# Kernel optimization log

Hardware: AMD Instinct MI355X
Metric: run time of the kernel (lower is better)

Reference implementation:

```python
import jax, jax.numpy as jnp
import numpy as np

# config (matches SS2Dv2 defaults: d_model=96, d_state=16, ssm_ratio=2.0, dt_rank=auto=6, k_group=4)
DM, DI, N, K, R = 96, 192, 16, 4, 6
BSZ, H_, W_ = 1, 56, 56


def setup_inputs() -> dict:
    key = jax.random.key(0)
    ks = jax.random.split(key, 8)
    return {
        "x": jax.random.normal(ks[0], (BSZ, H_, W_, DM), jnp.float32),
        "in_proj_w": jax.random.normal(ks[1], (2 * DI, DM), jnp.float32) / np.sqrt(DM).astype(np.float32),
        "conv_w": jax.random.normal(ks[2], (DI, 1, 3, 3), jnp.float32) * 0.1,
        "conv_b": jnp.zeros((DI,), jnp.float32),
        "x_proj_w": jax.random.normal(ks[3], (K, R + 2 * N, DI), jnp.float32) / np.sqrt(DI).astype(np.float32),
        "dt_projs_w": 0.1 * jax.random.uniform(ks[4], (K, DI, R), jnp.float32),
        "dt_projs_bias": 0.1 * jax.random.uniform(ks[5], (K, DI), jnp.float32),
        "A_logs": jnp.zeros((K * DI, N), jnp.float32),
        "Ds": jnp.ones((K * DI,), jnp.float32),
        "ln_w": jnp.ones((DI,), jnp.float32),
        "ln_b": jnp.zeros((DI,), jnp.float32),
        "out_proj_w": jax.random.normal(ks[6], (DM, DI), jnp.float32) / np.sqrt(DI).astype(np.float32),
    }


def _cross_scan(x):
    # x: (B, D, H, W) -> (B, 4, D, L); dirs: row-major, col-major, and their flips
    B, D, H, W = x.shape
    L = H * W
    x0 = x.reshape(B, D, L)
    x1 = jnp.swapaxes(x, 2, 3).reshape(B, D, L)
    return jnp.stack([x0, x1, x0[..., ::-1], x1[..., ::-1]], axis=1)


def _cross_merge(ys, H, W):
    # ys: (B, K, D, L) -> (B, D, L); invert each scan direction and sum
    B, Kk, D, L = ys.shape
    y0 = ys[:, 0]
    y2 = ys[:, 2][..., ::-1]
    y1 = jnp.swapaxes(ys[:, 1].reshape(B, D, W, H), 2, 3).reshape(B, D, L)
    y3 = jnp.swapaxes(ys[:, 3][..., ::-1].reshape(B, D, W, H), 2, 3).reshape(B, D, L)
    return y0 + y1 + y2 + y3


def _forward(x, in_proj_w, conv_w, conv_b, x_proj_w, dt_projs_w, dt_projs_bias,
             A_logs, Ds, ln_w, ln_b, out_proj_w):
    B, H, W, _ = x.shape
    L = H * W
    # in_proj + gate split (channel_first=False -> last dim)
    xz = jnp.einsum('bhwc,oc->bhwo', x, in_proj_w)
    xc, z = jnp.split(xz, 2, axis=-1)
    z = jax.nn.silu(z)
    # depthwise conv (NCHW)
    xc = jnp.transpose(xc, (0, 3, 1, 2))
    xc = jax.lax.conv_general_dilated(
        xc, conv_w, (1, 1), 'SAME', feature_group_count=DI,
        dimension_numbers=('NCHW', 'OIHW', 'NCHW')) + conv_b[None, :, None, None]
    xc = jax.nn.silu(xc)
    # 4-directional cross scan
    xs = _cross_scan(xc)  # (B,K,D,L)
    # grouped x_proj: per direction D -> R+2N
    x_dbl = jnp.einsum('bkdl,krd->bkrl', xs, x_proj_w)
    dts, Bs, Cs = jnp.split(x_dbl, [R, R + N], axis=2)  # (B,K,R,L),(B,K,N,L),(B,K,N,L)
    # grouped dt proj: per direction R -> D
    dts = jnp.einsum('bkrl,kdr->bkdl', dts, dt_projs_w)
    A = -jnp.exp(A_logs.astype(jnp.float32)).reshape(K, DI, N)
    delta = jax.nn.softplus(dts + dt_projs_bias[None, :, :, None])  # (B,K,D,L)
    # S6 selective scan: h_t = exp(delta*A)*h_{t-1} + delta*B*u, y_t = C.h_t + D*u
    dA = jnp.exp(jnp.einsum('bkdl,kdn->bkdln', delta, A))
    dBu = jnp.einsum('bkdl,bknl,bkdl->bkdln', delta, Bs, xs)

    def comb(e1, e2):
        a1, b1 = e1
        a2, b2 = e2
        return a2 * a1, a2 * b1 + b2

    _, h = jax.lax.associative_scan(comb, (dA, dBu), axis=3)  # (B,K,D,L,N)
    y = jnp.einsum('bkdln,bknl->bkdl', h, Cs) + Ds.reshape(K, DI)[None, :, :, None] * xs
    y = _cross_merge(y, H, W).reshape(B, DI, H, W)
    # out_norm: LayerNorm over channels (channel_first=False path)
    y = jnp.transpose(y, (0, 2, 3, 1))  # (B,H,W,D)
    mu = y.mean(-1, keepdims=True)
    var = ((y - mu) ** 2).mean(-1, keepdims=True)
    y = (y - mu) / jnp.sqrt(var + 1e-5) * ln_w + ln_b
    y = y * z
    return jnp.einsum('bhwd,od->bhwo', y, out_proj_w)


def reference(x, in_proj_w, conv_w, conv_b, x_proj_w, dt_projs_w, dt_projs_bias,
              A_logs, Ds, ln_w, ln_b, out_proj_w):
    return _forward(x, in_proj_w, conv_w, conv_b, x_proj_w, dt_projs_w, dt_projs_bias,
                    A_logs, Ds, ln_w, ln_b, out_proj_w)
```

## Files before the change

### kernel.cpp

```cpp
#include <hip/hip_runtime.h>
#include <hip/hip_bf16.h>
#include <math.h>

#define DM 96
#define DI 192
#define NS 16
#define KK 4
#define RR 6
#define HH 56
#define WW 56
#define LL (HH*WW)
#define RN (RR + 2*NS)
#define NCH 64
#define CLL (LL/NCH)

__device__ __forceinline__ float silu_f(float x) { return x / (1.f + __expf(-x)); }
__device__ __forceinline__ float softplus_f(float x) {
    return (x > 20.f) ? x : log1pf(__expf(x));
}

__global__ __launch_bounds__(256) void k_inproj(
        const float* __restrict__ x, const float* __restrict__ w,
        float* __restrict__ xc_t, float* __restrict__ z_nat) {
    __shared__ float xt[64 * 100];
    __shared__ float wt[32 * 100];
    const int l0 = blockIdx.x * 64;
    const int o0 = blockIdx.y * 32;
    const int tid = threadIdx.x;
    for (int i = tid; i < 64 * 96; i += 256) {
        int r = i / 96, c = i % 96;
        xt[r * 100 + c] = x[(size_t)(l0 + r) * DM + c];
    }
    for (int i = tid; i < 32 * 96; i += 256) {
        int r = i / 96, c = i % 96;
        wt[r * 100 + c] = w[(size_t)(o0 + r) * DM + c];
    }
    __syncthreads();
    const int tx = tid & 15, ty = tid >> 4;
    float acc[4][2] = {};
    for (int c = 0; c < 96; c += 4) {
        float4 av[4], bv[2];
#pragma unroll
        for (int i = 0; i < 4; ++i) av[i] = *(const float4*)&xt[(ty + 16 * i) * 100 + c];
#pragma unroll
        for (int j = 0; j < 2; ++j) bv[j] = *(const float4*)&wt[(tx + 16 * j) * 100 + c];
#pragma unroll
        for (int i = 0; i < 4; ++i)
#pragma unroll
            for (int j = 0; j < 2; ++j) {
                acc[i][j] = fmaf(av[i].x, bv[j].x, acc[i][j]);
                acc[i][j] = fmaf(av[i].y, bv[j].y, acc[i][j]);
                acc[i][j] = fmaf(av[i].z, bv[j].z, acc[i][j]);
                acc[i][j] = fmaf(av[i].w, bv[j].w, acc[i][j]);
            }
    }
    __syncthreads();
    float* ot = xt;
#pragma unroll
    for (int j = 0; j < 2; ++j)
#pragma unroll
        for (int i = 0; i < 4; ++i)
            ot[(tx + 16 * j) * 65 + (ty + 16 * i)] = acc[i][j];
    __syncthreads();
    if (o0 < DI) {
        for (int i = tid; i < 32 * 64; i += 256) {
            int ol = i >> 6, ll = i & 63;
            xc_t[(size_t)(o0 + ol) * LL + l0 + ll] = ot[ol * 65 + ll];
        }
    } else {
        for (int i = tid; i < 32 * 64; i += 256) {
            int ll = i >> 5, ol = i & 31;
            z_nat[(size_t)(l0 + ll) * DI + (o0 - DI) + ol] = silu_f(ot[ol * 65 + ll]);
        }
    }
}

__global__ __launch_bounds__(256) void k_convT(
        const float* __restrict__ xc_t, const float* __restrict__ cw,
        const float* __restrict__ cb, float* __restrict__ xconv, float* __restrict__ xs1) {
    __shared__ float in_s[16 * 56];
    __shared__ float out_s[14 * 57];
    const int d = blockIdx.x;
    const int h0 = blockIdx.y * 14;
    const int tid = threadIdx.x;
    const float* in = xc_t + (size_t)d * LL;
    for (int i = tid; i < 16 * 56; i += 256) {
        int r = i / 56 - 1 + h0;
        int cpos = i % 56;
        in_s[i] = (r >= 0 && r < HH) ? in[r * WW + cpos] : 0.f;
    }
    __syncthreads();
    const float b0 = cb[d];
    float w9[9];
#pragma unroll
    for (int i = 0; i < 9; ++i) w9[i] = cw[d * 9 + i];
    for (int i = tid; i < 14 * 56; i += 256) {
        int hh = i / 56, w = i % 56;
        float acc = b0;
#pragma unroll
        for (int di = 0; di < 3; ++di)
#pragma unroll
            for (int dj = 0; dj < 3; ++dj) {
                int w2 = w + dj - 1;
                if (w2 < 0 || w2 >= WW) continue;
                acc = fmaf(in_s[(hh + di) * 56 + w2], w9[di * 3 + dj], acc);
            }
        acc = silu_f(acc);
        xconv[(size_t)d * LL + (h0 + hh) * WW + w] = acc;
        out_s[hh * 57 + w] = acc;
    }
    __syncthreads();
    for (int i = tid; i < 14 * 56; i += 256) {
        int w = i / 14, hh = i % 14;
        xs1[(size_t)d * LL + w * HH + h0 + hh] = out_s[hh * 57 + w];
    }
}

__global__ __launch_bounds__(256) void k_xdblD(
        const float* __restrict__ xconv, const float* __restrict__ xs1,
        const float* __restrict__ pw, const float* __restrict__ dtw,
        const float* __restrict__ dtb,
        float* __restrict__ Bn, float* __restrict__ Cn, float* __restrict__ delta) {
    __shared__ float xt[DI * 32];
    __shared__ float wk_s[32 * DI];
    __shared__ float dtS[RR * 33];
    const int k = blockIdx.y;
    const int l0 = blockIdx.x * 32;
    const int tid = threadIdx.x;
    const float* in = (k & 1) ? xs1 : xconv;
    const float* wk = pw + (size_t)k * RN * DI;
    for (int i = tid; i < DI * 32; i += 256) {
        int d = i >> 5, lx = i & 31;
        xt[i] = in[(size_t)d * LL + l0 + lx];
    }
    {
        const float4* src = (const float4*)(wk + RR * DI);
        float4* dst = (float4*)wk_s;
        for (int i = tid; i < (32 * DI) / 4; i += 256) dst[i] = src[i];
    }
    __syncthreads();
    if (tid < RR * 32) {
        int r = tid >> 5, lx = tid & 31;
        const float* wr = wk + r * DI;
        float acc = 0.f;
#pragma unroll 8
        for (int d = 0; d < DI; ++d) acc = fmaf(xt[(d << 5) + lx], wr[d], acc);
        dtS[r * 33 + lx] = acc;
    }
    {
        const int sx = tid & 31, cg = tid >> 5;
        float acc4[4] = {};
        for (int d = 0; d < DI; d += 4) {
            float x0 = xt[(d + 0) * 32 + sx];
            float x1 = xt[(d + 1) * 32 + sx];
            float x2 = xt[(d + 2) * 32 + sx];
            float x3 = xt[(d + 3) * 32 + sx];
#pragma unroll
            for (int j = 0; j < 4; ++j) {
                float4 wv = *(const float4*)&wk_s[(cg + 8 * j) * DI + d];
                acc4[j] = fmaf(x0, wv.x, acc4[j]);
                acc4[j] = fmaf(x1, wv.y, acc4[j]);
                acc4[j] = fmaf(x2, wv.z, acc4[j]);
                acc4[j] = fmaf(x3, wv.w, acc4[j]);
            }
        }
        int s = l0 + sx;
#pragma unroll
        for (int j = 0; j < 4; ++j) {
            int col = cg + 8 * j;
            if (col < NS) Bn[((size_t)k * LL + s) * NS + col] = acc4[j];
            else          Cn[((size_t)k * LL + s) * NS + (col - NS)] = acc4[j];
        }
    }
    __syncthreads();
    for (int oi = tid; oi < DI * 32; oi += 256) {
        int d = oi >> 5, sl = oi & 31;
        int kd = k * DI + d;
        const float* wr = dtw + (size_t)kd * RR;
        float acc = dtb[kd];
#pragma unroll
        for (int r = 0; r < RR; ++r) acc = fmaf(dtS[r * 33 + sl], wr[r], acc);
        delta[(size_t)kd * LL + l0 + sl] = softplus_f(acc);
    }
}

template<int STP, bool TRANS>
__device__ __forceinline__ void scan_dir(
        const float* __restrict__ pd, const float* __restrict__ pu,
        const float* __restrict__ pB, const float* __restrict__ pC,
        float An, float Dv, int c, int n,
        float* __restrict__ sP, float* __restrict__ sH,
        float* __restrict__ yo0,
        float* __restrict__ ysm,
        int im0) {
    float sd = 0.f, h = 0.f;
#pragma unroll 7
    for (int tl = 0; tl < CLL; ++tl) {
        float dl = pd[STP * tl];
        float u  = pu[STP * tl];
        float Bv = pB[STP * NS * tl];
        float dA = __expf(dl * An);
        h = fmaf(dA, h, dl * Bv * u);
        sd += dl;
    }
    sP[c * NS + n] = __expf(sd * An);
    sH[c * NS + n] = h;
    __syncthreads();
    float hin = 0.f;
    for (int cc = 0; cc < c; ++cc)
        hin = fmaf(sP[cc * NS + n], hin, sH[cc * NS + n]);

    float h2 = hin;
    float yreg[4];
#pragma unroll 7
    for (int tl = 0; tl < CLL; ++tl) {
        float dl = pd[STP * tl];
        float u  = pu[STP * tl];
        float Bv = pB[STP * NS * tl];
        float Cv = pC[STP * NS * tl];
        float dA = __expf(dl * An);
        h2 = fmaf(dA, h2, dl * Bv * u);
        float acc = h2 * Cv;
        acc += __shfl_xor(acc, 8, 64);
        acc += __shfl_xor(acc, 4, 64);
        acc += __shfl_xor(acc, 2, 64);
        acc += __shfl_xor(acc, 1, 64);
        acc = fmaf(Dv, u, acc);
        if ((tl & 15) == n) yreg[tl >> 4] = acc;
    }
    if (!TRANS) {
#pragma unroll
        for (int j = 0; j < 3; ++j)
            yo0[STP * (j * 16 + n)] = yreg[j];
        if (n == 0)
            yo0[STP * 48] = yreg[3];
    } else {
#pragma unroll
        for (int j = 0; j < 3; ++j) {
            int im = im0 + STP * (j * 16 + n);
            int w = im / HH, hh = im - w * HH;
            ysm[hh * 57 + w] = yreg[j];
        }
        if (n == 0) {
            int im = im0 + STP * 48;
            int w = im / HH, hh = im - w * HH;
            ysm[hh * 57 + w] = yreg[3];
        }
    }
}

__global__ __launch_bounds__(1024) void k_scan(
        const float* __restrict__ delta, const float* __restrict__ Bn,
        const float* __restrict__ Cn,
        const float* __restrict__ xconv, const float* __restrict__ xs1,
        const float* __restrict__ A_logs, const float* __restrict__ Ds,
        float* __restrict__ y4) {
    __shared__ float sP[NCH * NS];
    __shared__ float sH[NCH * NS];
    __shared__ float ys[HH * 57];
    int b = blockIdx.x;
    int k = b / DI, d = b % DI;
    int tid = threadIdx.x;
    int c = tid >> 4, n = tid & 15;
    int kd = k * DI + d;
    float An = -__expf(A_logs[kd * NS + n]);
    float Dv = Ds[kd];
    const float* del = delta + (size_t)kd * LL;
    const float* uP  = ((k & 1) ? xs1 : xconv) + (size_t)d * LL;
    const float* Bb  = Bn + (size_t)k * LL * NS;
    const float* Cb  = Cn + (size_t)k * LL * NS;
    float* yo = y4 + (size_t)kd * LL;
    const int t0 = c * CLL;
    const int imF = t0;
    const int imR = LL - 1 - t0;
    if (k == 0) {
        scan_dir<1, false>(del + imF, uP + imF,
                           Bb + (size_t)imF * NS + n, Cb + (size_t)imF * NS + n,
                           An, Dv, c, n, sP, sH, yo + imF, nullptr, 0);
    } else if (k == 1) {
        scan_dir<1, true>(del + imF, uP + imF,
                          Bb + (size_t)imF * NS + n, Cb + (size_t)imF * NS + n,
                          An, Dv, c, n, sP, sH, nullptr, ys, imF);
    } else if (k == 2) {
        scan_dir<-1, false>(del + imR, uP + imR,
                            Bb + (size_t)imR * NS + n, Cb + (size_t)imR * NS + n,
                            An, Dv, c, n, sP, sH, yo + imR, nullptr, 0);
    } else {
        scan_dir<-1, true>(del + imR, uP + imR,
                           Bb + (size_t)imR * NS + n, Cb + (size_t)imR * NS + n,
                           An, Dv, c, n, sP, sH, nullptr, ys, imR);
    }
    if (k & 1) {
        __syncthreads();
        for (int p = tid; p < LL; p += 1024)
            yo[p] = ys[p + p / WW];
    }
}

__global__ __launch_bounds__(256) void k_lnout(
        const float* __restrict__ y4, const float* __restrict__ z_nat,
        const float* __restrict__ lnw, const float* __restrict__ lnb,
        const float* __restrict__ ow, float* __restrict__ out) {
    __shared__ float yv[32 * 196];
    __shared__ float ow_s[48 * 196];
    __shared__ float mean_s[32], inv_s[32];
    const int l0 = blockIdx.x * 32;
    const int pass = blockIdx.y;
    const int tid = threadIdx.x;
    for (int i = tid; i < DI * 32; i += 256) {
        int d = i >> 5, p = i & 31;
        size_t off = (size_t)d * LL + l0 + p;
        float v = y4[off]
                + y4[(size_t)DI * LL + off]
                + y4[(size_t)(2 * DI) * LL + off]
                + y4[(size_t)(3 * DI) * LL + off];
        yv[p * 196 + d] = v;
    }
    __syncthreads();
    {
        int p = tid >> 3, e = tid & 7;
        float s1 = 0.f;
#pragma unroll
        for (int m = 0; m < 24; ++m) s1 += yv[p * 196 + e + 8 * m];
        s1 += __shfl_xor(s1, 4, 64);
        s1 += __shfl_xor(s1, 2, 64);
        s1 += __shfl_xor(s1, 1, 64);
        float mean = s1 * (1.f / DI);
        float s2 = 0.f;
#pragma unroll
        for (int m = 0; m < 24; ++m) {
            float dv = yv[p * 196 + e + 8 * m] - mean;
            s2 = fmaf(dv, dv, s2);
        }
        s2 += __shfl_xor(s2, 4, 64);
        s2 += __shfl_xor(s2, 2, 64);
        s2 += __shfl_xor(s2, 1, 64);
        if (e == 0) {
            mean_s[p] = mean;
            inv_s[p] = rsqrtf(s2 * (1.f / DI) + 1e-5f);
        }
    }
    __syncthreads();
    for (int i = tid; i < DI * 32; i += 256) {
        int p = i / DI, d = i % DI;
        float yn = (yv[p * 196 + d] - mean_s[p]) * inv_s[p] * lnw[d] + lnb[d];
        yv[p * 196 + d] = yn * z_nat[(size_t)(l0 + p) * DI + d];
    }
    for (int i = tid; i < 48 * DI; i += 256) {
        int o = i / DI, dd = i % DI;
        ow_s[o * 196 + dd] = ow[(size_t)(pass * 48 + o) * DI + dd];
    }
    __syncthreads();
    const int ty = tid >> 4, tx = tid & 15;
    float acc[2][3] = {};
    for (int dd = 0; dd < DI; dd += 4) {
        float4 a0 = *(const float4*)&yv[(ty * 2 + 0) * 196 + dd];
        float4 a1 = *(const float4*)&yv[(ty * 2 + 1) * 196 + dd];
#pragma unroll
        for (int j = 0; j < 3; ++j) {
            float4 bv = *(const float4*)&ow_s[(tx + 16 * j) * 196 + dd];
            acc[0][j] += a0.x * bv.x + a0.y * bv.y + a0.z * bv.z + a0.w * bv.w;
            acc[1][j] += a1.x * bv.x + a1.y * bv.y + a1.z * bv.z + a1.w * bv.w;
        }
    }
#pragma unroll
    for (int il = 0; il < 2; ++il)
#pragma unroll
        for (int j = 0; j < 3; ++j)
            out[(size_t)(l0 + ty * 2 + il) * DM + pass * 48 + tx + 16 * j] = acc[il][j];
}

extern "C" void kernel_launch(void* const* d_in, const int* in_sizes, int n_in,
                              void* d_out, int out_size, void* d_ws, size_t ws_size,
                              hipStream_t stream) {
    const float* x    = (const float*)d_in[0];
    const float* ipw  = (const float*)d_in[1];
    const float* cw   = (const float*)d_in[2];
    const float* cb   = (const float*)d_in[3];
    const float* xpw  = (const float*)d_in[4];
    const float* dtw  = (const float*)d_in[5];
    const float* dtb  = (const float*)d_in[6];
    const float* alog = (const float*)d_in[7];
    const float* Dsp  = (const float*)d_in[8];
    const float* lnw  = (const float*)d_in[9];
    const float* lnb  = (const float*)d_in[10];
    const float* ow   = (const float*)d_in[11];
    float* out = (float*)d_out;

    float* ws     = (float*)d_ws;
    float* xc_t   = ws;
    float* z_nat  = xc_t + DI * LL;
    float* xconv  = z_nat + DI * LL;
    float* xs1    = xconv + DI * LL;
    float* Bn     = xs1 + DI * LL;
    float* Cn     = Bn + (size_t)KK * LL * NS;
    float* delta  = Cn + (size_t)KK * LL * NS;
    float* y4     = delta + (size_t)KK * DI * LL;

    k_inproj <<<dim3(LL / 64, 12), 256, 0, stream>>>(x, ipw, xc_t, z_nat);
    k_convT  <<<dim3(DI, 4), 256, 0, stream>>>(xc_t, cw, cb, xconv, xs1);
    k_xdblD  <<<dim3(LL / 32, KK), 256, 0, stream>>>(xconv, xs1, xpw, dtw, dtb, Bn, Cn, delta);
    k_scan   <<<KK * DI, 1024, 0, stream>>>(delta, Bn, Cn, xconv, xs1, alog, Dsp, y4);
    k_lnout  <<<dim3(LL / 32, 2), 256, 0, stream>>>(y4, z_nat, lnw, lnb, ow, out);
}
```

Baseline: 187.7 us.

## Store delta/B/C chunk-major in scan order and vectorize global loads

```diff
diff --git a/kernel.cpp b/kernel.cpp
--- a/kernel.cpp
+++ b/kernel.cpp
@@ -12,7 +12,8 @@
 #define LL (HH*WW)
 #define RN (RR + 2*NS)
 #define NCH 64
-#define CLL (LL/NCH)
+#define CLL 49
+#define CPAD 52
 
 __device__ __forceinline__ float silu_f(float x) { return x / (1.f + __expf(-x)); }
 __device__ __forceinline__ float softplus_f(float x) {
@@ -27,13 +28,13 @@
     const int l0 = blockIdx.x * 64;
     const int o0 = blockIdx.y * 32;
     const int tid = threadIdx.x;
-    for (int i = tid; i < 64 * 96; i += 256) {
-        int r = i / 96, c = i % 96;
-        xt[r * 100 + c] = x[(size_t)(l0 + r) * DM + c];
-    }
-    for (int i = tid; i < 32 * 96; i += 256) {
-        int r = i / 96, c = i % 96;
-        wt[r * 100 + c] = w[(size_t)(o0 + r) * DM + c];
+    for (int i = tid; i < 64 * 24; i += 256) {
+        int r = i / 24, q = i % 24;
+        *(float4*)&xt[r * 100 + 4 * q] = *(const float4*)&x[(size_t)(l0 + r) * DM + 4 * q];
+    }
+    for (int i = tid; i < 32 * 24; i += 256) {
+        int r = i / 24, q = i % 24;
+        *(float4*)&wt[r * 100 + 4 * q] = *(const float4*)&w[(size_t)(o0 + r) * DM + 4 * q];
     }
     __syncthreads();
     const int tx = tid & 15, ty = tid >> 4;
@@ -84,10 +85,12 @@
     const int h0 = blockIdx.y * 14;
     const int tid = threadIdx.x;
     const float* in = xc_t + (size_t)d * LL;
-    for (int i = tid; i < 16 * 56; i += 256) {
-        int r = i / 56 - 1 + h0;
-        int cpos = i % 56;
-        in_s[i] = (r >= 0 && r < HH) ? in[r * WW + cpos] : 0.f;
+    for (int i = tid; i < 16 * 14; i += 256) {
+        int row = i / 14, q = i % 14;
+        int r = row - 1 + h0;
+        float4 v = make_float4(0.f, 0.f, 0.f, 0.f);
+        if (r >= 0 && r < HH) v = *(const float4*)&in[r * WW + 4 * q];
+        *(float4*)&in_s[row * 56 + 4 * q] = v;
     }
     __syncthreads();
     const float b0 = cb[d];
@@ -120,7 +123,7 @@
         const float* __restrict__ xconv, const float* __restrict__ xs1,
         const float* __restrict__ pw, const float* __restrict__ dtw,
         const float* __restrict__ dtb,
-        float* __restrict__ Bn, float* __restrict__ Cn, float* __restrict__ delta) {
+        float* __restrict__ Bt, float* __restrict__ Ct, float* __restrict__ delta_cm) {
     __shared__ float xt[DI * 32];
     __shared__ float wk_s[32 * DI];
     __shared__ float dtS[RR * 33];
@@ -129,9 +132,9 @@
     const int tid = threadIdx.x;
     const float* in = (k & 1) ? xs1 : xconv;
     const float* wk = pw + (size_t)k * RN * DI;
-    for (int i = tid; i < DI * 32; i += 256) {
-        int d = i >> 5, lx = i & 31;
-        xt[i] = in[(size_t)d * LL + l0 + lx];
+    for (int i = tid; i < DI * 8; i += 256) {
+        int d = i >> 3, q = i & 7;
+        *(float4*)&xt[(d << 5) + 4 * q] = *(const float4*)&in[(size_t)d * LL + l0 + 4 * q];
     }
     {
         const float4* src = (const float4*)(wk + RR * DI);
@@ -165,11 +168,14 @@
             }
         }
         int s = l0 + sx;
+        int jt = (k < 2) ? s : (LL - 1 - s);
+        int c = jt / CLL, tw = jt - c * CLL;
+        size_t base = ((size_t)k * NCH + c) * NS;
 #pragma unroll
         for (int j = 0; j < 4; ++j) {
             int col = cg + 8 * j;
-            if (col < NS) Bn[((size_t)k * LL + s) * NS + col] = acc4[j];
-            else          Cn[((size_t)k * LL + s) * NS + (col - NS)] = acc4[j];
+            if (col < NS) Bt[(base + col) * CPAD + tw] = acc4[j];
+            else          Ct[(base + (col - NS)) * CPAD + tw] = acc4[j];
         }
     }
     __syncthreads();
@@ -180,13 +186,16 @@
         float acc = dtb[kd];
 #pragma unroll
         for (int r = 0; r < RR; ++r) acc = fmaf(dtS[r * 33 + sl], wr[r], acc);
-        delta[(size_t)kd * LL + l0 + sl] = softplus_f(acc);
+        int s = l0 + sl;
+        int jt = (k < 2) ? s : (LL - 1 - s);
+        int c = jt / CLL, tw = jt - c * CLL;
+        delta_cm[((size_t)kd * NCH + c) * CPAD + tw] = softplus_f(acc);
     }
 }
 
 template<int STP, bool TRANS>
 __device__ __forceinline__ void scan_dir(
-        const float* __restrict__ pd, const float* __restrict__ pu,
+        const float* __restrict__ pdel, const float* __restrict__ pu,
         const float* __restrict__ pB, const float* __restrict__ pC,
         float An, float Dv, int c, int n,
         float* __restrict__ sP, float* __restrict__ sH,
@@ -194,11 +203,24 @@
         float* __restrict__ ysm,
         int im0) {
     float sd = 0.f, h = 0.f;
-#pragma unroll 7
-    for (int tl = 0; tl < CLL; ++tl) {
-        float dl = pd[STP * tl];
-        float u  = pu[STP * tl];
-        float Bv = pB[STP * NS * tl];
+#pragma unroll
+    for (int g = 0; g < 12; ++g) {
+        float4 d4 = *(const float4*)(pdel + 4 * g);
+        float4 B4 = *(const float4*)(pB + 4 * g);
+        float uu[4];
+#pragma unroll
+        for (int j = 0; j < 4; ++j) uu[j] = pu[STP * (4 * g + j)];
+#pragma unroll
+        for (int j = 0; j < 4; ++j) {
+            float dl = ((const float*)&d4)[j];
+            float Bv = ((const float*)&B4)[j];
+            float dA = __expf(dl * An);
+            h = fmaf(dA, h, dl * Bv * uu[j]);
+            sd += dl;
+        }
+    }
+    {
+        float dl = pdel[48], Bv = pB[48], u = pu[STP * 48];
         float dA = __expf(dl * An);
         h = fmaf(dA, h, dl * Bv * u);
         sd += dl;
@@ -212,12 +234,33 @@
 
     float h2 = hin;
     float yreg[4];
-#pragma unroll 7
-    for (int tl = 0; tl < CLL; ++tl) {
-        float dl = pd[STP * tl];
-        float u  = pu[STP * tl];
-        float Bv = pB[STP * NS * tl];
-        float Cv = pC[STP * NS * tl];
+#pragma unroll
+    for (int g = 0; g < 12; ++g) {
+        float4 d4 = *(const float4*)(pdel + 4 * g);
+        float4 B4 = *(const float4*)(pB + 4 * g);
+        float4 C4 = *(const float4*)(pC + 4 * g);
+        float uu[4];
+#pragma unroll
+        for (int j = 0; j < 4; ++j) uu[j] = pu[STP * (4 * g + j)];
+#pragma unroll
+        for (int j = 0; j < 4; ++j) {
+            float dl = ((const float*)&d4)[j];
+            float Bv = ((const float*)&B4)[j];
+            float Cv = ((const float*)&C4)[j];
+            float dA = __expf(dl * An);
+            h2 = fmaf(dA, h2, dl * Bv * uu[j]);
+            float acc = h2 * Cv;
+            acc += __shfl_xor(acc, 8, 64);
+            acc += __shfl_xor(acc, 4, 64);
+            acc += __shfl_xor(acc, 2, 64);
+            acc += __shfl_xor(acc, 1, 64);
+            acc = fmaf(Dv, uu[j], acc);
+            int tl = 4 * g + j;
+            if ((tl & 15) == n) yreg[tl >> 4] = acc;
+        }
+    }
+    {
+        float dl = pdel[48], Bv = pB[48], Cv = pC[48], u = pu[STP * 48];
         float dA = __expf(dl * An);
         h2 = fmaf(dA, h2, dl * Bv * u);
         float acc = h2 * Cv;
@@ -226,7 +269,7 @@
         acc += __shfl_xor(acc, 2, 64);
         acc += __shfl_xor(acc, 1, 64);
         acc = fmaf(Dv, u, acc);
-        if ((tl & 15) == n) yreg[tl >> 4] = acc;
+        if (n == 0) yreg[3] = acc;
     }
     if (!TRANS) {
 #pragma unroll
@@ -250,8 +293,8 @@
 }
 
 __global__ __launch_bounds__(1024) void k_scan(
-        const float* __restrict__ delta, const float* __restrict__ Bn,
-        const float* __restrict__ Cn,
+        const float* __restrict__ delta_cm, const float* __restrict__ Bt,
+        const float* __restrict__ Ct,
         const float* __restrict__ xconv, const float* __restrict__ xs1,
         const float* __restrict__ A_logs, const float* __restrict__ Ds,
         float* __restrict__ y4) {
@@ -265,30 +308,26 @@
     int kd = k * DI + d;
     float An = -__expf(A_logs[kd * NS + n]);
     float Dv = Ds[kd];
-    const float* del = delta + (size_t)kd * LL;
-    const float* uP  = ((k & 1) ? xs1 : xconv) + (size_t)d * LL;
-    const float* Bb  = Bn + (size_t)k * LL * NS;
-    const float* Cb  = Cn + (size_t)k * LL * NS;
+    const float* pdel = delta_cm + ((size_t)kd * NCH + c) * CPAD;
+    const float* pB   = Bt + (((size_t)k * NCH + c) * NS + n) * CPAD;
+    const float* pC   = Ct + (((size_t)k * NCH + c) * NS + n) * CPAD;
+    const float* uP   = ((k & 1) ? xs1 : xconv) + (size_t)d * LL;
     float* yo = y4 + (size_t)kd * LL;
     const int t0 = c * CLL;
     const int imF = t0;
     const int imR = LL - 1 - t0;
     if (k == 0) {
-        scan_dir<1, false>(del + imF, uP + imF,
-                           Bb + (size_t)imF * NS + n, Cb + (size_t)imF * NS + n,
-                           An, Dv, c, n, sP, sH, yo + imF, nullptr, 0);
+        scan_dir<1, false>(pdel, uP + imF, pB, pC, An, Dv, c, n, sP, sH,
+                           yo + imF, nullptr, 0);
     } else if (k == 1) {
-        scan_dir<1, true>(del + imF, uP + imF,
-                          Bb + (size_t)imF * NS + n, Cb + (size_t)imF * NS + n,
-                          An, Dv, c, n, sP, sH, nullptr, ys, imF);
+        scan_dir<1, true>(pdel, uP + imF, pB, pC, An, Dv, c, n, sP, sH,
+                          nullptr, ys, imF);
     } else if (k == 2) {
-        scan_dir<-1, false>(del + imR, uP + imR,
-                            Bb + (size_t)imR * NS + n, Cb + (size_t)imR * NS + n,
-                            An, Dv, c, n, sP, sH, yo + imR, nullptr, 0);
+        scan_dir<-1, false>(pdel, uP + imR, pB, pC, An, Dv, c, n, sP, sH,
+                            yo + imR, nullptr, 0);
     } else {
-        scan_dir<-1, true>(del + imR, uP + imR,
-                           Bb + (size_t)imR * NS + n, Cb + (size_t)imR * NS + n,
-                           An, Dv, c, n, sP, sH, nullptr, ys, imR);
+        scan_dir<-1, true>(pdel, uP + imR, pB, pC, An, Dv, c, n, sP, sH,
+                           nullptr, ys, imR);
     }
     if (k & 1) {
         __syncthreads();
@@ -307,14 +346,18 @@
     const int l0 = blockIdx.x * 32;
     const int pass = blockIdx.y;
     const int tid = threadIdx.x;
-    for (int i = tid; i < DI * 32; i += 256) {
-        int d = i >> 5, p = i & 31;
-        size_t off = (size_t)d * LL + l0 + p;
-        float v = y4[off]
-                + y4[(size_t)DI * LL + off]
-                + y4[(size_t)(2 * DI) * LL + off]
-                + y4[(size_t)(3 * DI) * LL + off];
-        yv[p * 196 + d] = v;
+    for (int i = tid; i < DI * 8; i += 256) {
+        int d = i >> 3, q = i & 7;
+        size_t off = (size_t)d * LL + l0 + 4 * q;
+        float4 a = *(const float4*)&y4[off];
+        float4 b = *(const float4*)&y4[(size_t)DI * LL + off];
+        float4 c2 = *(const float4*)&y4[(size_t)(2 * DI) * LL + off];
+        float4 e = *(const float4*)&y4[(size_t)(3 * DI) * LL + off];
+        int p = 4 * q;
+        yv[(p + 0) * 196 + d] = a.x + b.x + c2.x + e.x;
+        yv[(p + 1) * 196 + d] = a.y + b.y + c2.y + e.y;
+        yv[(p + 2) * 196 + d] = a.z + b.z + c2.z + e.z;
+        yv[(p + 3) * 196 + d] = a.w + b.w + c2.w + e.w;
     }
     __syncthreads();
     {
@@ -341,14 +384,23 @@
         }
     }
     __syncthreads();
-    for (int i = tid; i < DI * 32; i += 256) {
-        int p = i / DI, d = i % DI;
-        float yn = (yv[p * 196 + d] - mean_s[p]) * inv_s[p] * lnw[d] + lnb[d];
-        yv[p * 196 + d] = yn * z_nat[(size_t)(l0 + p) * DI + d];
-    }
-    for (int i = tid; i < 48 * DI; i += 256) {
-        int o = i / DI, dd = i % DI;
-        ow_s[o * 196 + dd] = ow[(size_t)(pass * 48 + o) * DI + dd];
+    for (int i = tid; i < 32 * 48; i += 256) {
+        int p = i / 48, q = i % 48;
+        float4 z4 = *(const float4*)&z_nat[(size_t)(l0 + p) * DI + 4 * q];
+        float4 w4 = *(const float4*)&lnw[4 * q];
+        float4 b4 = *(const float4*)&lnb[4 * q];
+        float4 yy = *(const float4*)&yv[p * 196 + 4 * q];
+        float m = mean_s[p], iv = inv_s[p];
+        yy.x = ((yy.x - m) * iv * w4.x + b4.x) * z4.x;
+        yy.y = ((yy.y - m) * iv * w4.y + b4.y) * z4.y;
+        yy.z = ((yy.z - m) * iv * w4.z + b4.z) * z4.z;
+        yy.w = ((yy.w - m) * iv * w4.w + b4.w) * z4.w;
+        *(float4*)&yv[p * 196 + 4 * q] = yy;
+    }
+    for (int i = tid; i < 48 * 48; i += 256) {
+        int o = i / 48, q = i % 48;
+        *(float4*)&ow_s[o * 196 + 4 * q] =
+            *(const float4*)&ow[(size_t)(pass * 48 + o) * DI + 4 * q];
     }
     __syncthreads();
     const int ty = tid >> 4, tx = tid & 15;
@@ -387,19 +439,19 @@
     const float* ow   = (const float*)d_in[11];
     float* out = (float*)d_out;
 
-    float* ws     = (float*)d_ws;
-    float* xc_t   = ws;
-    float* z_nat  = xc_t + DI * LL;
-    float* xconv  = z_nat + DI * LL;
-    float* xs1    = xconv + DI * LL;
-    float* Bn     = xs1 + DI * LL;
-    float* Cn     = Bn + (size_t)KK * LL * NS;
-    float* delta  = Cn + (size_t)KK * LL * NS;
-    float* y4     = delta + (size_t)KK * DI * LL;
+    float* ws       = (float*)d_ws;
+    float* xc_t     = ws;
+    float* z_nat    = xc_t + DI * LL;
+    float* xconv    = z_nat + DI * LL;
+    float* xs1      = xconv + DI * LL;
+    float* Bt       = xs1 + DI * LL;
+    float* Ct       = Bt + (size_t)KK * NCH * NS * CPAD;
+    float* delta_cm = Ct + (size_t)KK * NCH * NS * CPAD;
+    float* y4       = delta_cm + (size_t)KK * DI * NCH * CPAD;
 
     k_inproj <<<dim3(LL / 64, 12), 256, 0, stream>>>(x, ipw, xc_t, z_nat);
     k_convT  <<<dim3(DI, 4), 256, 0, stream>>>(xc_t, cw, cb, xconv, xs1);
-    k_xdblD  <<<dim3(LL / 32, KK), 256, 0, stream>>>(xconv, xs1, xpw, dtw, dtb, Bn, Cn, delta);
-    k_scan   <<<KK * DI, 1024, 0, stream>>>(delta, Bn, Cn, xconv, xs1, alog, Dsp, y4);
+    k_xdblD  <<<dim3(LL / 32, KK), 256, 0, stream>>>(xconv, xs1, xpw, dtw, dtb, Bt, Ct, delta_cm);
+    k_scan   <<<KK * DI, 1024, 0, stream>>>(delta_cm, Bt, Ct, xconv, xs1, alog, Dsp, y4);
     k_lnout  <<<dim3(LL / 32, 2), 256, 0, stream>>>(y4, z_nat, lnw, lnb, ow, out);
 }
```

Result: slower. 235.9 us (+25.7%).
